# Optimization experiments

Measured on AMD Instinct MI355X. Metric: run time of the kernel, lower is better.

## Reference

```python
import jax, jax.numpy as jnp
import numpy as np

D_MODEL = 1024
D_INTERNAL = 1024
B, T = 4, 2048
ROPE_BASE = 10000.0


def _rotate_half(x):
    h = x.shape[-1] // 2
    return jnp.concatenate([-x[..., h:], x[..., :h]], axis=-1)


def _justnorm(x):
    return x / jnp.linalg.norm(x, axis=-1, keepdims=True)


def setup_inputs() -> dict:
    key = jax.random.key(0)
    k1, k2 = jax.random.split(key)
    stdev = 1.0 / (D_MODEL + D_INTERNAL) ** 0.5
    qkv_w = jax.random.uniform(k1, (3 * D_INTERNAL, D_MODEL), minval=-stdev, maxval=stdev, dtype=jnp.float32)
    qkv_w = _justnorm(qkv_w)  # source normalizes qkv rows at init
    sqk = (D_MODEL ** -0.5) * jnp.ones((D_INTERNAL,), dtype=jnp.float32)  # sqk_init_scaling * ones
    input_vecs = jax.random.normal(k2, (B, T, D_MODEL), dtype=jnp.float32)
    return {"input_vecs": input_vecs, "qkv_w": qkv_w, "sqk": sqk}


def reference(input_vecs, qkv_w, sqk):
    d_model = input_vecs.shape[-1]
    d_int = qkv_w.shape[0] // 3
    t_len = input_vecs.shape[-2]

    # QKV projection: F.linear(x, W) == x @ W.T
    qkv = jnp.einsum('btc,dc->btd', input_vecs, qkv_w)
    Q, K, V = jnp.split(qkv, 3, axis=-1)  # each [B, T, d_int]

    # Rotary embeddings over full d_int
    inv_freq = 1.0 / (ROPE_BASE ** (jnp.arange(0, d_int, 2, dtype=jnp.float32) / d_int))
    t = jnp.arange(t_len, dtype=jnp.float32)
    freqs = t[:, None] * inv_freq[None, :]              # [T, d_int/2]
    emb = jnp.concatenate([freqs, freqs], axis=-1)      # [T, d_int]
    cos, sin = jnp.cos(emb), jnp.sin(emb)
    Q = Q * cos + _rotate_half(Q) * sin
    K = K * cos + _rotate_half(K) * sin

    # L2 QK-norm with learned per-channel scale (sqk * (1.0 / sqk_init_scaling))
    sqk_eff = sqk * (d_model ** 0.5)
    Q = _justnorm(Q) * sqk_eff
    K = _justnorm(K) * sqk_eff

    # SDPA, eval path: causal, dropout=0, scale = C ** 0.5
    scale = d_model ** 0.5
    scores = jnp.einsum('bqd,bkd->bqk', Q, K) * scale   # [B, T, T]
    causal = jnp.tril(jnp.ones((t_len, t_len), dtype=bool))
    scores = jnp.where(causal[None, :, :], scores, -jnp.inf)
    attn = jax.nn.softmax(scores, axis=-1)
    out = jnp.einsum('bqk,bkd->bqd', attn, V)
    return out
```

## Files before the change

kernel.cpp:

```cpp
#include <hip/hip_runtime.h>

typedef unsigned short u16;
typedef short s16x8 __attribute__((ext_vector_type(8)));
typedef float f32x4 __attribute__((ext_vector_type(4)));

__device__ __forceinline__ u16 f2bf(float f) {
    union { float f; unsigned u; } v; v.f = f;
    unsigned r = v.u + 0x7FFFu + ((v.u >> 16) & 1u);
    return (u16)(r >> 16);
}
__device__ __forceinline__ float bf2f(u16 h) {
    union { unsigned u; float f; } v; v.u = ((unsigned)h) << 16;
    return v.f;
}
__device__ __forceinline__ u16 f2h(float f) {
    _Float16 h = (_Float16)f;
    union { _Float16 h; u16 u; } v; v.h = h; return v.u;
}
__device__ __forceinline__ float h2f(u16 u) {
    union { u16 u; _Float16 h; } v; v.u = u; return (float)v.h;
}

__device__ __forceinline__ void gl_lds16(const u16* g, u16* l) {
    __builtin_amdgcn_global_load_lds(
        (const __attribute__((address_space(1))) void*)g,
        (__attribute__((address_space(3))) void*)l,
        16, 0, 0);
}

__device__ __forceinline__ s16x8 ldfrag(const u16* base, int row, int kk, int fq) {
    int cb = ((kk << 6) + (fq << 4)) ^ ((row & 7) << 4);
    return *reinterpret_cast<const s16x8*>(base + row * 64 + (cb >> 1));
}

#define MFMA16(a, b, c) __builtin_amdgcn_mfma_f32_16x16x32_bf16((a), (b), (c), 0, 0, 0)

__global__ __launch_bounds__(256)
void prep(const float* __restrict__ x, const float* __restrict__ w,
          u16* __restrict__ xb, u16* __restrict__ wb, u16* __restrict__ trig) {
    const int bid = blockIdx.x;
    if (bid < 2048) {
        int i = (bid * 256 + threadIdx.x) * 4;
        const int stride = 2048 * 256 * 4;
        for (; i < 8192 * 1024; i += stride) {
            float4 v = *reinterpret_cast<const float4*>(x + i);
            ushort4 o;
            o.x = f2bf(v.x); o.y = f2bf(v.y); o.z = f2bf(v.z); o.w = f2bf(v.w);
            *reinterpret_cast<ushort4*>(xb + i) = o;
        }
    } else if (bid < 2816) {
        int i = ((bid - 2048) * 256 + threadIdx.x) * 4;
        const int stride = 768 * 256 * 4;
        for (; i < 3072 * 1024; i += stride) {
            float4 v = *reinterpret_cast<const float4*>(w + i);
            ushort4 o;
            o.x = f2bf(v.x); o.y = f2bf(v.y); o.z = f2bf(v.z); o.w = f2bf(v.w);
            *reinterpret_cast<ushort4*>(wb + i) = o;
        }
    } else {
        const int t = bid - 2816;
        const float L = 0.025952563241307517f;
        u16* row = trig + (size_t)t * 1024;
#pragma unroll
        for (int i = 0; i < 2; ++i) {
            int d = threadIdx.x + i * 256;
            float invf = exp2f(-(float)d * L);
            float ang = (float)t * invf;
            float s, c;
            sincosf(ang, &s, &c);
            row[d] = f2h(c);
            row[512 + d] = f2h(s);
        }
    }
}

template <int MODE, typename CT>
__global__ __launch_bounds__(256, 2)
void gemm_bt(const u16* __restrict__ A, const u16* __restrict__ B, CT* __restrict__ C,
             u16* __restrict__ VT, float* __restrict__ psum, const float* __restrict__ rowinv,
             int K, int lda, int ldb, int ldc, long sA, long sB, long sC) {
    int bx, by, bz;
    if (MODE == 0) {
        int bid = blockIdx.x;
        int xcd = bid & 7, idx = bid >> 3;
        int r = idx >> 6, w2 = idx & 63;
        bx = r * 8 + (w2 & 7);
        by = xcd * 8 + (w2 >> 3);
        bz = 0;
    } else {
        bx = blockIdx.x; by = blockIdx.y; bz = blockIdx.z;
    }
    if (MODE == 1 && bx > by) return;
    if (MODE == 2) { bz = blockIdx.y & 3; by = 15 - (int)(blockIdx.y >> 2); }
    A += (size_t)bz * sA; B += (size_t)bz * sB; C += (size_t)bz * sC;
    int kend = K;
    if (MODE == 2) { int kl = (by + 1) * 128; kend = kl < K ? kl : K; }
    const int NT = kend >> 6;

    __shared__ u16 lds[32768];

    const int tid  = threadIdx.x;
    const int lane = tid & 63;
    const int wave = tid >> 6;
    const int wr = (wave >> 1) * 64;
    const int wc = (wave & 1) * 64;
    const int fr = lane & 15;
    const int fq = lane >> 4;
    const int tm = by * 128, tn = bx * 128;

    const int srow = tid >> 3;
    const int gco  = (((tid & 7) ^ (srow & 7)) << 3);
    const u16* aR[4]; const u16* bR[4];
#pragma unroll
    for (int j = 0; j < 4; ++j) {
        aR[j] = A + (size_t)(tm + j * 32 + srow) * lda + gco;
        bR[j] = B + (size_t)(tn + j * 32 + srow) * ldb + gco;
    }

#define STAGE(b2, k0) do {                                                        \
    _Pragma("unroll") for (int j = 0; j < 4; ++j)                                 \
        gl_lds16(aR[j] + (k0), lds + (b2) * 16384 + j * 2048 + tid * 8);          \
    _Pragma("unroll") for (int j = 0; j < 4; ++j)                                 \
        gl_lds16(bR[j] + (k0), lds + (b2) * 16384 + 8192 + j * 2048 + tid * 8);   \
  } while (0)

    f32x4 acc[4][4];
#pragma unroll
    for (int m = 0; m < 4; ++m)
#pragma unroll
        for (int n = 0; n < 4; ++n) acc[m][n] = {0.f, 0.f, 0.f, 0.f};

    STAGE(0, 0);
    if (NT > 1) STAGE(1, 64);

    for (int t = 0; t < NT; ++t) {
        const int buf = t & 1;
        if (t + 1 < NT) { asm volatile("s_waitcnt vmcnt(8)" ::: "memory"); }
        else            { asm volatile("s_waitcnt vmcnt(0)" ::: "memory"); }
        __builtin_amdgcn_s_barrier();
        __builtin_amdgcn_sched_barrier(0);

        const u16* Ab = lds + buf * 16384;
        const u16* Bb = Ab + 8192;
        s16x8 bf0[4], bf1[4];
#pragma unroll
        for (int n = 0; n < 4; ++n) {
            bf0[n] = ldfrag(Bb, wc + n * 16 + fr, 0, fq);
            bf1[n] = ldfrag(Bb, wc + n * 16 + fr, 1, fq);
        }
        __builtin_amdgcn_s_setprio(1);
#pragma unroll
        for (int m = 0; m < 4; ++m) {
            s16x8 a0 = ldfrag(Ab, wr + m * 16 + fr, 0, fq);
            s16x8 a1 = ldfrag(Ab, wr + m * 16 + fr, 1, fq);
#pragma unroll
            for (int n = 0; n < 4; ++n) {
                acc[m][n] = MFMA16(a0, bf0[n], acc[m][n]);
                acc[m][n] = MFMA16(a1, bf1[n], acc[m][n]);
            }
        }
        __builtin_amdgcn_s_setprio(0);
        __builtin_amdgcn_sched_barrier(0);
        __builtin_amdgcn_s_barrier();
        if (t + 2 < NT) STAGE(buf, (t + 2) << 6);
    }
#undef STAGE

    if (MODE == 0 && tn >= 2048) {
#pragma unroll
        for (int m = 0; m < 4; ++m)
#pragma unroll
            for (int n = 0; n < 4; ++n)
#pragma unroll
                for (int r = 0; r < 4; ++r) {
                    int row = tm + wr + m * 16 + fq * 4 + r;
                    int col = tn + wc + n * 16 + fr;
                    VT[((size_t)(row >> 11)) * 2097152 + (size_t)(col - 2048) * 2048 + (row & 2047)]
                        = f2bf(acc[m][n][r]);
                }
    } else if (MODE == 1) {
        u16* P = (u16*)C;
#pragma unroll
        for (int m = 0; m < 4; ++m) {
#pragma unroll
            for (int r = 0; r < 4; ++r) {
                int row = tm + wr + m * 16 + fq * 4 + r;
                float rs = 0.f;
#pragma unroll
                for (int n = 0; n < 4; ++n) {
                    int col = tn + wc + n * 16 + fr;
                    float p = (col <= row) ? __expf(32.f * acc[m][n][r] - 32.f) : 0.f;
                    u16 pb = f2bf(p);
                    P[(size_t)row * 2048 + col] = pb;
                    rs += bf2f(pb);
                }
                rs += __shfl_xor(rs, 1);
                rs += __shfl_xor(rs, 2);
                rs += __shfl_xor(rs, 4);
                rs += __shfl_xor(rs, 8);
                if (fr == 0)
                    psum[((size_t)bz * 32 + bx * 2 + (wave & 1)) * 2048 + row] = rs;
            }
        }
    } else if (MODE == 2) {
#pragma unroll
        for (int m = 0; m < 4; ++m) {
#pragma unroll
            for (int r = 0; r < 4; ++r) {
                int row = tm + wr + m * 16 + fq * 4 + r;
                float inv = rowinv[(size_t)bz * 2048 + row];
#pragma unroll
                for (int n = 0; n < 4; ++n) {
                    int col = tn + wc + n * 16 + fr;
                    C[(size_t)row * ldc + col] = acc[m][n][r] * inv;
                }
            }
        }
    } else {
#pragma unroll
        for (int m = 0; m < 4; ++m)
#pragma unroll
            for (int n = 0; n < 4; ++n)
#pragma unroll
                for (int r = 0; r < 4; ++r) {
                    int row = tm + wr + m * 16 + fq * 4 + r;
                    int col = tn + wc + n * 16 + fr;
                    C[(size_t)row * ldc + col] = (CT)f2bf(acc[m][n][r]);
                }
    }
}

__global__ __launch_bounds__(256)
void row_reduce(const float* __restrict__ psum, float* __restrict__ rowinv) {
    const int r = blockIdx.x * 256 + threadIdx.x;
    const int b = blockIdx.y;
    const int nslots = 2 * ((r >> 7) + 1);
    float s = 0.f;
    for (int j = 0; j < nslots; ++j)
        s += psum[((size_t)b * 32 + j) * 2048 + r];
    rowinv[(size_t)b * 2048 + r] = 1.f / s;
}

__global__ __launch_bounds__(256)
void rope_norm(u16* __restrict__ qk, const float* __restrict__ sqk,
               const u16* __restrict__ trig) {
    const int row = blockIdx.x;
    const int t = row & 2047;
    u16* qp = qk + (size_t)row * 2048;
    u16* kp = qp + 1024;
    const u16* tb = trig + (size_t)t * 1024;
    const int d = threadIdx.x << 1;

    union U2 { uint u; u16 h[2]; };
    U2 qc0, qc1, kc0, kc1, cc, ss;
    qc0.u = *reinterpret_cast<const uint*>(qp + d);
    qc1.u = *reinterpret_cast<const uint*>(qp + 512 + d);
    kc0.u = *reinterpret_cast<const uint*>(kp + d);
    kc1.u = *reinterpret_cast<const uint*>(kp + 512 + d);
    cc.u  = *reinterpret_cast<const uint*>(tb + d);
    ss.u  = *reinterpret_cast<const uint*>(tb + 512 + d);

    float nq0[2], nq1[2], nk0[2], nk1[2];
    float ssq_q = 0.f, ssq_k = 0.f;
#pragma unroll
    for (int j = 0; j < 2; ++j) {
        float c = h2f(cc.h[j]), s = h2f(ss.h[j]);
        float q0 = bf2f(qc0.h[j]), q1 = bf2f(qc1.h[j]);
        float k0 = bf2f(kc0.h[j]), k1 = bf2f(kc1.h[j]);
        nq0[j] = q0 * c - q1 * s;
        nq1[j] = q1 * c + q0 * s;
        nk0[j] = k0 * c - k1 * s;
        nk1[j] = k1 * c + k0 * s;
        ssq_q += nq0[j] * nq0[j] + nq1[j] * nq1[j];
        ssq_k += nk0[j] * nk0[j] + nk1[j] * nk1[j];
    }

#pragma unroll
    for (int off = 32; off; off >>= 1) {
        ssq_q += __shfl_xor(ssq_q, off);
        ssq_k += __shfl_xor(ssq_k, off);
    }
    __shared__ float red[8];
    int wave = threadIdx.x >> 6, lane = threadIdx.x & 63;
    if (lane == 0) { red[wave] = ssq_q; red[4 + wave] = ssq_k; }
    __syncthreads();
    float rq = rsqrtf(red[0] + red[1] + red[2] + red[3]);
    float rk = rsqrtf(red[4] + red[5] + red[6] + red[7]);

    float2 sq0 = *reinterpret_cast<const float2*>(sqk + d);
    float2 sq1 = *reinterpret_cast<const float2*>(sqk + 512 + d);
    float s0[2] = {sq0.x * 32.f, sq0.y * 32.f};
    float s1[2] = {sq1.x * 32.f, sq1.y * 32.f};

    U2 oq0, oq1, ok0, ok1;
#pragma unroll
    for (int j = 0; j < 2; ++j) {
        oq0.h[j] = f2bf(nq0[j] * rq * s0[j]);
        oq1.h[j] = f2bf(nq1[j] * rq * s1[j]);
        ok0.h[j] = f2bf(nk0[j] * rk * s0[j]);
        ok1.h[j] = f2bf(nk1[j] * rk * s1[j]);
    }
    *reinterpret_cast<uint*>(qp + d)       = oq0.u;
    *reinterpret_cast<uint*>(qp + 512 + d) = oq1.u;
    *reinterpret_cast<uint*>(kp + d)       = ok0.u;
    *reinterpret_cast<uint*>(kp + 512 + d) = ok1.u;
}

extern "C" void kernel_launch(void* const* d_in, const int* in_sizes, int n_in,
                              void* d_out, int out_size, void* d_ws, size_t ws_size,
                              hipStream_t stream) {
    const float* x   = (const float*)d_in[0];
    const float* w   = (const float*)d_in[1];
    const float* sqk = (const float*)d_in[2];
    float* out = (float*)d_out;

    const size_t SZ_XB  = (size_t)8192 * 1024 * 2;
    const size_t SZ_WB  = (size_t)3072 * 1024 * 2;
    const size_t SZ_QK  = (size_t)8192 * 2048 * 2;
    const size_t SZ_VT  = (size_t)4 * 1024 * 2048 * 2;
    const size_t SZ_P   = (size_t)4 * 2048 * 2048 * 2;
    const size_t SZ_TR  = (size_t)2048 * 1024 * 2;
    const size_t SZ_PS  = (size_t)4 * 32 * 2048 * 4;
    const size_t SZ_RI  = (size_t)4 * 2048 * 4;
    if (ws_size < SZ_XB + SZ_WB + SZ_QK + SZ_VT + SZ_P + SZ_TR + SZ_PS + SZ_RI) return;

    char* ws = (char*)d_ws;
    u16*   xb     = (u16*)ws;   ws += SZ_XB;
    u16*   wb     = (u16*)ws;   ws += SZ_WB;
    u16*   qk     = (u16*)ws;   ws += SZ_QK;
    u16*   VT     = (u16*)ws;   ws += SZ_VT;
    u16*   P      = (u16*)ws;   ws += SZ_P;
    u16*   trig   = (u16*)ws;   ws += SZ_TR;
    float* psum   = (float*)ws; ws += SZ_PS;
    float* rowinv = (float*)ws;

    prep<<<4864, 256, 0, stream>>>(x, w, xb, wb, trig);

    gemm_bt<0, u16><<<dim3(1536, 1, 1), 256, 0, stream>>>(
        xb, wb, qk, VT, nullptr, nullptr, 1024, 1024, 1024, 2048, 0, 0, 0);

    rope_norm<<<8192, 256, 0, stream>>>(qk, sqk, trig);

    gemm_bt<1, u16><<<dim3(16, 16, 4), 256, 0, stream>>>(
        qk, qk + 1024, P, nullptr, psum, nullptr, 1024, 2048, 2048, 2048,
        (long)2048 * 2048, (long)2048 * 2048, (long)2048 * 2048);

    row_reduce<<<dim3(8, 4), 256, 0, stream>>>(psum, rowinv);

    gemm_bt<2, float><<<dim3(8, 64, 1), 256, 0, stream>>>(
        P, VT, out, nullptr, nullptr, rowinv, 2048, 2048, 2048, 1024,
        (long)2048 * 2048, (long)1024 * 2048, (long)2048 * 1024);
}
```

Baseline: 158.9 us.

## Compact causal grid with XCD-aware mapping and fuse row reduction into PV GEMM

After: 146.1 us, median of 2. -8.1%, faster.

```diff
diff --git a/kernel.cpp b/kernel.cpp
--- a/kernel.cpp
+++ b/kernel.cpp
@@ -77,7 +77,7 @@
 template <int MODE, typename CT>
 __global__ __launch_bounds__(256, 2)
 void gemm_bt(const u16* __restrict__ A, const u16* __restrict__ B, CT* __restrict__ C,
-             u16* __restrict__ VT, float* __restrict__ psum, const float* __restrict__ rowinv,
+             u16* __restrict__ VT, float* __restrict__ psum,
              int K, int lda, int ldb, int ldc, long sA, long sB, long sC) {
     int bx, by, bz;
     if (MODE == 0) {
@@ -87,11 +87,23 @@
         bx = r * 8 + (w2 & 7);
         by = xcd * 8 + (w2 >> 3);
         bz = 0;
+    } else if (MODE == 1) {
+        int bid = blockIdx.x;
+        int xcd = bid & 7;
+        bz = xcd >> 1;
+        int j = (xcd & 1) * 68 + (bid >> 3);
+        by = (int)((sqrtf(8.f * j + 1.f) - 1.f) * 0.5f);
+        while ((by + 1) * (by + 2) / 2 <= j) ++by;
+        while (by * (by + 1) / 2 > j) --by;
+        bx = j - by * (by + 1) / 2;
     } else {
-        bx = blockIdx.x; by = blockIdx.y; bz = blockIdx.z;
-    }
-    if (MODE == 1 && bx > by) return;
-    if (MODE == 2) { bz = blockIdx.y & 3; by = 15 - (int)(blockIdx.y >> 2); }
+        int bid = blockIdx.x;
+        int xcd = bid & 7;
+        bz = xcd >> 1;
+        int j = (xcd & 1) * 64 + (bid >> 3);
+        by = 15 - (j >> 3);
+        bx = j & 7;
+    }
     A += (size_t)bz * sA; B += (size_t)bz * sB; C += (size_t)bz * sC;
     int kend = K;
     if (MODE == 2) { int kl = (by + 1) * 128; kend = kl < K ? kl : K; }
@@ -203,12 +215,23 @@
             }
         }
     } else if (MODE == 2) {
+        float* rinv = (float*)lds;
+        if (tid < 128) {
+            int row = tm + tid;
+            int ns = 2 * (by + 1);
+            float s = 0.f;
+            for (int j = 0; j < ns; ++j)
+                s += psum[((size_t)bz * 32 + j) * 2048 + row];
+            rinv[tid] = 1.f / s;
+        }
+        __syncthreads();
 #pragma unroll
         for (int m = 0; m < 4; ++m) {
 #pragma unroll
             for (int r = 0; r < 4; ++r) {
-                int row = tm + wr + m * 16 + fq * 4 + r;
-                float inv = rowinv[(size_t)bz * 2048 + row];
+                int lrow = wr + m * 16 + fq * 4 + r;
+                float inv = rinv[lrow];
+                int row = tm + lrow;
 #pragma unroll
                 for (int n = 0; n < 4; ++n) {
                     int col = tn + wc + n * 16 + fr;
@@ -228,17 +251,6 @@
                     C[(size_t)row * ldc + col] = (CT)f2bf(acc[m][n][r]);
                 }
     }
-}
-
-__global__ __launch_bounds__(256)
-void row_reduce(const float* __restrict__ psum, float* __restrict__ rowinv) {
-    const int r = blockIdx.x * 256 + threadIdx.x;
-    const int b = blockIdx.y;
-    const int nslots = 2 * ((r >> 7) + 1);
-    float s = 0.f;
-    for (int j = 0; j < nslots; ++j)
-        s += psum[((size_t)b * 32 + j) * 2048 + r];
-    rowinv[(size_t)b * 2048 + r] = 1.f / s;
 }
 
 __global__ __launch_bounds__(256)
@@ -321,33 +333,29 @@
     const size_t SZ_P   = (size_t)4 * 2048 * 2048 * 2;
     const size_t SZ_TR  = (size_t)2048 * 1024 * 2;
     const size_t SZ_PS  = (size_t)4 * 32 * 2048 * 4;
-    const size_t SZ_RI  = (size_t)4 * 2048 * 4;
-    if (ws_size < SZ_XB + SZ_WB + SZ_QK + SZ_VT + SZ_P + SZ_TR + SZ_PS + SZ_RI) return;
+    if (ws_size < SZ_XB + SZ_WB + SZ_QK + SZ_VT + SZ_P + SZ_TR + SZ_PS) return;
 
     char* ws = (char*)d_ws;
-    u16*   xb     = (u16*)ws;   ws += SZ_XB;
-    u16*   wb     = (u16*)ws;   ws += SZ_WB;
-    u16*   qk     = (u16*)ws;   ws += SZ_QK;
-    u16*   VT     = (u16*)ws;   ws += SZ_VT;
-    u16*   P      = (u16*)ws;   ws += SZ_P;
-    u16*   trig   = (u16*)ws;   ws += SZ_TR;
-    float* psum   = (float*)ws; ws += SZ_PS;
-    float* rowinv = (float*)ws;
+    u16*   xb   = (u16*)ws;   ws += SZ_XB;
+    u16*   wb   = (u16*)ws;   ws += SZ_WB;
+    u16*   qk   = (u16*)ws;   ws += SZ_QK;
+    u16*   VT   = (u16*)ws;   ws += SZ_VT;
+    u16*   P    = (u16*)ws;   ws += SZ_P;
+    u16*   trig = (u16*)ws;   ws += SZ_TR;
+    float* psum = (float*)ws;
 
     prep<<<4864, 256, 0, stream>>>(x, w, xb, wb, trig);
 
     gemm_bt<0, u16><<<dim3(1536, 1, 1), 256, 0, stream>>>(
-        xb, wb, qk, VT, nullptr, nullptr, 1024, 1024, 1024, 2048, 0, 0, 0);
+        xb, wb, qk, VT, nullptr, 1024, 1024, 1024, 2048, 0, 0, 0);
 
     rope_norm<<<8192, 256, 0, stream>>>(qk, sqk, trig);
 
-    gemm_bt<1, u16><<<dim3(16, 16, 4), 256, 0, stream>>>(
-        qk, qk + 1024, P, nullptr, psum, nullptr, 1024, 2048, 2048, 2048,
+    gemm_bt<1, u16><<<dim3(544, 1, 1), 256, 0, stream>>>(
+        qk, qk + 1024, P, nullptr, psum, 1024, 2048, 2048, 2048,
         (long)2048 * 2048, (long)2048 * 2048, (long)2048 * 2048);
 
-    row_reduce<<<dim3(8, 4), 256, 0, stream>>>(psum, rowinv);
-
-    gemm_bt<2, float><<<dim3(8, 64, 1), 256, 0, stream>>>(
-        P, VT, out, nullptr, nullptr, rowinv, 2048, 2048, 2048, 1024,
+    gemm_bt<2, float><<<dim3(512, 1, 1), 256, 0, stream>>>(
+        P, VT, out, nullptr, psum, 2048, 2048, 2048, 1024,
         (long)2048 * 2048, (long)1024 * 2048, (long)2048 * 1024);
 }
```
